# Performance work log

Measured on AMD Instinct MI355X. Metric: run time of the kernel, lower is better.

Reference implementation:

```python
import jax, jax.numpy as jnp
import numpy as np

NUM_EMBEDDINGS = 1024
EMBEDDING_DIM = 64
COMMITMENT_COST = 0.25
N_TOKENS = 262144


def setup_inputs() -> dict:
    key = jax.random.key(0)
    k1, k2 = jax.random.split(key)
    inputs = jax.random.normal(k1, (N_TOKENS, EMBEDDING_DIM), dtype=jnp.float32)
    # torch init: uniform(-1/K, 1/K)
    lim = 1.0 / NUM_EMBEDDINGS
    codebook = jax.random.uniform(k2, (NUM_EMBEDDINGS, EMBEDDING_DIM),
                                  dtype=jnp.float32, minval=-lim, maxval=lim)
    return {"inputs": inputs, "codebook": codebook}


def reference(inputs, codebook):
    # inputs: [N, D] flat tokens, codebook: [K, D]
    x = inputs.reshape(-1, EMBEDDING_DIM)
    distances = (jnp.sum(x * x, axis=1, keepdims=True)
                 + jnp.sum(codebook * codebook, axis=1)
                 - 2.0 * jnp.matmul(x, codebook.T))
    encoding_indices = jnp.argmin(distances, axis=1)[:, None]  # [N, 1]
    # one-hot @ codebook == gather of nearest code vectors
    quantized = codebook[encoding_indices[:, 0]]  # [N, D]
    e_latent_loss = jnp.mean((jax.lax.stop_gradient(quantized) - x) ** 2)
    q_latent_loss = jnp.mean((quantized - jax.lax.stop_gradient(x)) ** 2)
    loss = q_latent_loss + COMMITMENT_COST * e_latent_loss
    # straight-through estimator
    quantized = x + jax.lax.stop_gradient(quantized - x)
    return quantized, loss, encoding_indices
```

## Files before the change

kernel.cpp:

```cpp
#include <hip/hip_runtime.h>
#include <math.h>

#define NTOK   262144
#define DIM    64
#define NCODE  1024
#define LOSSOFF (NTOK*DIM)
#define IDXOFF  (NTOK*DIM + 1)

#define MARGIN 4e-5f
#define RCAP   65536

#define OFF_BC     0
#define OFF_CBHI   1024
#define OFF_CBMID  33792
#define OFF_RCNT   66560
#define OFF_CORR   66561
#define OFF_RLIST  66562
#define OFF_BLK    132098
#define WS_FLOATS  134146

typedef __attribute__((ext_vector_type(8))) short short8;
typedef __attribute__((ext_vector_type(4))) float f32x4;

__device__ __forceinline__ ushort bf16rn(float f) {
    unsigned u = __float_as_uint(f);
    return (ushort)((u + 0x7fffu + ((u >> 16) & 1u)) >> 16);
}
__device__ __forceinline__ float bf16tof(ushort h) {
    return __uint_as_float(((unsigned)h) << 16);
}

__global__ __launch_bounds__(256) void vq_prep_cb(const float* __restrict__ cb,
                                                  float* __restrict__ ws) {
    int c = blockIdx.x * 256 + threadIdx.x;
    if (c == 0) { ((int*)ws)[OFF_RCNT] = 0; ws[OFF_CORR] = 0.f; }
    if (c >= NCODE) return;
    ushort* cbh = (ushort*)(ws + OFF_CBHI);
    ushort* cbm = (ushort*)(ws + OFF_CBMID);
    const float4* p = (const float4*)(cb + (size_t)c * DIM);
    float a0 = 0.f, a1 = 0.f, a2 = 0.f, a3 = 0.f;
#pragma unroll
    for (int i = 0; i < 16; i++) {
        float4 v = p[i];
        a0 = fmaf(v.x, v.x, a0); a1 = fmaf(v.y, v.y, a1);
        a2 = fmaf(v.z, v.z, a2); a3 = fmaf(v.w, v.w, a3);
        ushort4 h, m;
        h.x = bf16rn(v.x); m.x = bf16rn(v.x - bf16tof(h.x));
        h.y = bf16rn(v.y); m.y = bf16rn(v.y - bf16tof(h.y));
        h.z = bf16rn(v.z); m.z = bf16rn(v.z - bf16tof(h.z));
        h.w = bf16rn(v.w); m.w = bf16rn(v.w - bf16tof(h.w));
        ((ushort4*)(cbh + (size_t)c * 64))[i] = h;
        ((ushort4*)(cbm + (size_t)c * 64))[i] = m;
    }
    ws[OFF_BC + c] = (a0 + a1) + (a2 + a3);
}

__global__ __launch_bounds__(256)
__attribute__((amdgpu_waves_per_eu(3)))
void vq_mfma(const float* __restrict__ x,
             const float* __restrict__ cbf,
             float* __restrict__ out,
             float* __restrict__ ws) {
    __shared__ uint4 smem[8][256];
    __shared__ int idxs[128];
    __shared__ float red[4];
    const float* Bc = ws + OFF_BC;
    const ushort* cbh = (const ushort*)(ws + OFF_CBHI);
    const ushort* cbm = (const ushort*)(ws + OFF_CBMID);

    int tid = threadIdx.x, lane = tid & 63, wv = tid >> 6;
    int col = lane & 15, q = lane >> 4, q4 = q * 4;
    int tokb = blockIdx.x * 128 + wv * 32;

    short8 Xhi[2][2], Xmid[2][2];
#pragma unroll
    for (int tt = 0; tt < 2; ++tt) {
        int token = tokb + tt * 16 + col;
        const float* xr = x + (size_t)token * 64;
#pragma unroll
        for (int s = 0; s < 2; ++s) {
            float4 v0 = *(const float4*)(xr + s * 32 + q * 8);
            float4 v1 = *(const float4*)(xr + s * 32 + q * 8 + 4);
            float vv[8] = {v0.x, v0.y, v0.z, v0.w, v1.x, v1.y, v1.z, v1.w};
            short8 hv, mv;
#pragma unroll
            for (int j = 0; j < 8; ++j) {
                ushort h = bf16rn(vv[j]);
                float r = vv[j] - bf16tof(h);
                hv[j] = (short)h; mv[j] = (short)bf16rn(r);
            }
            Xhi[tt][s] = hv; Xmid[tt][s] = mv;
        }
    }

    float best[2][4], sec[2][4];
    int bbase[2][4];
#pragma unroll
    for (int tt = 0; tt < 2; ++tt)
#pragma unroll
        for (int rr = 0; rr < 4; ++rr) {
            best[tt][rr] = 3.4e38f; sec[tt][rr] = 3.4e38f; bbase[tt][rr] = 0;
        }

    int chunk = tid >> 7, e = tid & 127, scode = e >> 3, g = e & 7;
    const ushort* sb0 = (chunk ? cbm : cbh) + (size_t)scode * 64 + g * 8;
    int woff = chunk * 128 + scode * 8 + (g ^ (scode & 7));
    int ro_h0 = col * 8 + ((0 + q) ^ (col & 7));
    int ro_h1 = col * 8 + ((4 + q) ^ (col & 7));
    int ro_m0 = 128 + col * 8 + ((0 + q) ^ (col & 7));
    int ro_m1 = 128 + col * 8 + ((4 + q) ^ (col & 7));

    uint4 r0 = *(const uint4*)(sb0);
    uint4 r1 = *(const uint4*)(sb0 + 1024);
    uint4 r2 = *(const uint4*)(sb0 + 2048);
    uint4 r3 = *(const uint4*)(sb0 + 3072);
    smem[0][woff] = r0; smem[1][woff] = r1;
    smem[2][woff] = r2; smem[3][woff] = r3;
    r0 = *(const uint4*)(sb0 + 4096);
    r1 = *(const uint4*)(sb0 + 5120);
    r2 = *(const uint4*)(sb0 + 6144);
    r3 = *(const uint4*)(sb0 + 7168);
    __syncthreads();

    for (int rd = 0; rd < 16; ++rd) {
        int base = (rd & 1) << 2;
        int nb = 4 - base;
        if (rd < 15) {
            smem[nb + 0][woff] = r0; smem[nb + 1][woff] = r1;
            smem[nb + 2][woff] = r2; smem[nb + 3][woff] = r3;
            if (rd < 14) {
                const ushort* ld = sb0 + (size_t)(rd + 2) * 4096;
                r0 = *(const uint4*)(ld);
                r1 = *(const uint4*)(ld + 1024);
                r2 = *(const uint4*)(ld + 2048);
                r3 = *(const uint4*)(ld + 3072);
            }
        }
#pragma unroll
        for (int sub = 0; sub < 4; ++sub) {
            int c0 = (rd * 4 + sub) * 16;
            float4 bq = *(const float4*)(Bc + c0 + q4);
            short8 Ah0 = *(const short8*)&smem[base + sub][ro_h0];
            short8 Ah1 = *(const short8*)&smem[base + sub][ro_h1];
            short8 Am0 = *(const short8*)&smem[base + sub][ro_m0];
            short8 Am1 = *(const short8*)&smem[base + sub][ro_m1];
            int bv = c0 + q4;
            float bqv[4] = {bq.x, bq.y, bq.z, bq.w};
#pragma unroll
            for (int tt = 0; tt < 2; ++tt) {
                f32x4 acc = {0.f, 0.f, 0.f, 0.f};
                acc = __builtin_amdgcn_mfma_f32_16x16x32_bf16(Ah0, Xhi[tt][0], acc, 0, 0, 0);
                acc = __builtin_amdgcn_mfma_f32_16x16x32_bf16(Ah1, Xhi[tt][1], acc, 0, 0, 0);
                acc = __builtin_amdgcn_mfma_f32_16x16x32_bf16(Ah0, Xmid[tt][0], acc, 0, 0, 0);
                acc = __builtin_amdgcn_mfma_f32_16x16x32_bf16(Ah1, Xmid[tt][1], acc, 0, 0, 0);
                acc = __builtin_amdgcn_mfma_f32_16x16x32_bf16(Am0, Xhi[tt][0], acc, 0, 0, 0);
                acc = __builtin_amdgcn_mfma_f32_16x16x32_bf16(Am1, Xhi[tt][1], acc, 0, 0, 0);
#pragma unroll
                for (int rr = 0; rr < 4; ++rr) {
                    float d = fmaf(-2.f, acc[rr], bqv[rr]);
                    bool lt = d < best[tt][rr];
                    sec[tt][rr] = __builtin_amdgcn_fmed3f(d, best[tt][rr], sec[tt][rr]);
                    best[tt][rr] = fminf(best[tt][rr], d);
                    bbase[tt][rr] = lt ? bv : bbase[tt][rr];
                }
            }
        }
        __syncthreads();
    }

#pragma unroll
    for (int tt = 0; tt < 2; ++tt) {
        float b = best[tt][0], s2 = sec[tt][0];
        int bi = bbase[tt][0];
#pragma unroll
        for (int rr = 1; rr < 4; ++rr) {
            float ob = best[tt][rr];
            int oi = bbase[tt][rr] + rr;
            s2 = fminf(fminf(s2, sec[tt][rr]), fmaxf(b, ob));
            bool lt2 = (ob < b) || (ob == b && oi < bi);
            b = lt2 ? ob : b; bi = lt2 ? oi : bi;
        }
#pragma unroll
        for (int off = 16; off <= 32; off <<= 1) {
            float ob = __shfl_xor(b, off, 64);
            float os = __shfl_xor(s2, off, 64);
            int   oi = __shfl_xor(bi, off, 64);
            s2 = fminf(fminf(s2, os), fmaxf(b, ob));
            bool lt = (ob < b) || (ob == b && oi < bi);
            b = lt ? ob : b; bi = lt ? oi : bi;
        }
        if (lane < 16) {
            int token = tokb + tt * 16 + lane;
            out[IDXOFF + token] = (float)bi;
            idxs[wv * 32 + tt * 16 + lane] = bi;
            if (s2 - b < MARGIN) {
                int pos = atomicAdd((int*)ws + OFF_RCNT, 1);
                if (pos < RCAP) ((int*)ws)[OFF_RLIST + pos] = token;
            }
        }
    }
    __syncthreads();

    float se = 0.f;
    int tokb0 = blockIdx.x * 128;
#pragma unroll
    for (int i = 0; i < 8; ++i) {
        int gi = i * 256 + tid;
        int tok = gi >> 4, qd = gi & 15;
        int ci = idxs[tok];
        float4 xvv = *(const float4*)(x + (size_t)(tokb0 + tok) * 64 + qd * 4);
        float4 qv = *(const float4*)(cbf + (size_t)ci * 64 + qd * 4);
        float d0 = qv.x - xvv.x, d1 = qv.y - xvv.y;
        float d2 = qv.z - xvv.z, d3 = qv.w - xvv.w;
        float4 o;
        o.x = xvv.x + d0; o.y = xvv.y + d1; o.z = xvv.z + d2; o.w = xvv.w + d3;
        *(float4*)(out + (size_t)(tokb0 + tok) * 64 + qd * 4) = o;
        se += d0 * d0 + d1 * d1 + d2 * d2 + d3 * d3;
    }
    for (int off = 32; off; off >>= 1) se += __shfl_down(se, off, 64);
    if (lane == 0) red[wv] = se;
    __syncthreads();
    if (tid == 0) ws[OFF_BLK + blockIdx.x] = (red[0] + red[1]) + (red[2] + red[3]);
}

__global__ __launch_bounds__(256) void vq_refine(const float* __restrict__ x,
                                                 const float* __restrict__ cb,
                                                 float* __restrict__ out,
                                                 float* __restrict__ ws) {
    __shared__ float ctile[128][64];
    __shared__ float xs[8][64];
    __shared__ float As[8];
    __shared__ int   tokid[8], oidx[8], nidx[8];
    __shared__ unsigned long long rkeys[8][128];
    __shared__ float dred[4];

    int cnt = min(((int*)ws)[OFF_RCNT], RCAP);
    if (cnt <= 0) return;
    int ngroups = (cnt + 7) >> 3;
    int tid = threadIdx.x;
    int code = tid & 127, th = tid >> 7;

    for (int grp = blockIdx.x; grp < ngroups; grp += gridDim.x) {
        if (tid < 8) {
            int i = grp * 8 + tid;
            int t = ((int*)ws)[OFF_RLIST + min(i, cnt - 1)];
            tokid[tid] = t;
            oidx[tid] = (int)out[IDXOFF + t];
        }
        __syncthreads();
#pragma unroll
        for (int it = 0; it < 2; ++it) {
            int idx = it * 256 + tid;
            xs[idx >> 6][idx & 63] = x[(size_t)tokid[idx >> 6] * 64 + (idx & 63)];
        }
        __syncthreads();
        if (tid < 8) {
            float a0 = 0.f, a1 = 0.f, a2 = 0.f, a3 = 0.f;
#pragma unroll
            for (int kc = 0; kc < 16; ++kc) {
                float4 xk = *(const float4*)(xs[tid] + kc * 4);
                a0 = fmaf(xk.x, xk.x, a0); a1 = fmaf(xk.y, xk.y, a1);
                a2 = fmaf(xk.z, xk.z, a2); a3 = fmaf(xk.w, xk.w, a3);
            }
            As[tid] = (a0 + a1) + (a2 + a3);
        }

        unsigned long long bk[4] = {~0ull, ~0ull, ~0ull, ~0ull};
        int tb = th * 4;

        for (int pass = 0; pass < 8; ++pass) {
            int cbase = pass * 128;
            __syncthreads();
#pragma unroll
            for (int it = 0; it < 8; ++it) {
                int gi = it * 256 + tid;
                int cc = gi >> 4, qq = gi & 15;
                float4 v = *(const float4*)(cb + (size_t)(cbase + cc) * 64 + qq * 4);
                *(float4*)&ctile[cc][(qq ^ (cc & 15)) * 4] = v;
            }
            __syncthreads();

            float p0 = 0.f, p1 = 0.f, p2 = 0.f, p3 = 0.f;
#pragma unroll
            for (int qq = 0; qq < 16; ++qq) {
                float4 cv = *(const float4*)&ctile[code][(qq ^ (code & 15)) * 4];
                float4 x0 = *(const float4*)(xs[tb + 0] + qq * 4);
                float4 x1 = *(const float4*)(xs[tb + 1] + qq * 4);
                float4 x2 = *(const float4*)(xs[tb + 2] + qq * 4);
                float4 x3 = *(const float4*)(xs[tb + 3] + qq * 4);
                p0 = fmaf(x0.x, cv.x, p0); p0 = fmaf(x0.y, cv.y, p0);
                p0 = fmaf(x0.z, cv.z, p0); p0 = fmaf(x0.w, cv.w, p0);
                p1 = fmaf(x1.x, cv.x, p1); p1 = fmaf(x1.y, cv.y, p1);
                p1 = fmaf(x1.z, cv.z, p1); p1 = fmaf(x1.w, cv.w, p1);
                p2 = fmaf(x2.x, cv.x, p2); p2 = fmaf(x2.y, cv.y, p2);
                p2 = fmaf(x2.z, cv.z, p2); p2 = fmaf(x2.w, cv.w, p2);
                p3 = fmaf(x3.x, cv.x, p3); p3 = fmaf(x3.y, cv.y, p3);
                p3 = fmaf(x3.z, cv.z, p3); p3 = fmaf(x3.w, cv.w, p3);
            }
            float bn = ws[OFF_BC + cbase + code];
            int gcode = cbase + code;
            float pv[4] = {p0, p1, p2, p3};
#pragma unroll
            for (int j = 0; j < 4; ++j) {
                float s = As[tb + j] + bn;
                float d = fmaf(-2.0f, pv[j], s);
                unsigned long long key =
                    (((unsigned long long)__float_as_uint(d)) << 32) | (unsigned)gcode;
                bk[j] = min(bk[j], key);
            }
        }
        __syncthreads();
#pragma unroll
        for (int j = 0; j < 4; ++j) rkeys[tb + j][code] = bk[j];
        __syncthreads();

        int wv2 = tid >> 6, lane = tid & 63;
#pragma unroll
        for (int u = 0; u < 2; ++u) {
            int tt = wv2 * 2 + u;
            unsigned long long k = min(rkeys[tt][lane], rkeys[tt][lane + 64]);
#pragma unroll
            for (int off = 32; off; off >>= 1)
                k = min(k, (unsigned long long)__shfl_xor((long long)k, off, 64));
            if (lane == 0) {
                int ni = (int)(unsigned)(k & 0xffffffffull);
                nidx[tt] = ni;
                if (grp * 8 + tt < cnt) out[IDXOFF + tokid[tt]] = (float)ni;
            }
        }
        __syncthreads();

        float delta = 0.f;
        {
            int tok = tid >> 5, e2 = (tid & 31) * 2;
            if (grp * 8 + tok < cnt) {
                int nw = nidx[tok], od = oidx[tok];
                if (nw != od) {
                    float x0 = xs[tok][e2], x1 = xs[tok][e2 + 1];
                    float qn0 = cb[(size_t)nw * 64 + e2], qn1 = cb[(size_t)nw * 64 + e2 + 1];
                    float qo0 = cb[(size_t)od * 64 + e2], qo1 = cb[(size_t)od * 64 + e2 + 1];
                    float dn0 = qn0 - x0, dn1 = qn1 - x1;
                    float do0 = qo0 - x0, do1 = qo1 - x1;
                    out[(size_t)tokid[tok] * 64 + e2]     = x0 + dn0;
                    out[(size_t)tokid[tok] * 64 + e2 + 1] = x1 + dn1;
                    delta = (dn0 * dn0 + dn1 * dn1) - (do0 * do0 + do1 * do1);
                }
            }
        }
        for (int off = 32; off; off >>= 1) delta += __shfl_down(delta, off, 64);
        if ((tid & 63) == 0) dred[tid >> 6] = delta;
        __syncthreads();
        if (tid == 0) {
            float dsum = (dred[0] + dred[1]) + (dred[2] + dred[3]);
            if (dsum != 0.f) atomicAdd(ws + OFF_CORR, dsum);
        }
        __syncthreads();
    }
}

__global__ __launch_bounds__(256) void vq_loss2(float* __restrict__ out,
                                                const float* __restrict__ ws) {
    const float* blk = ws + OFF_BLK;
    __shared__ double sd[256];
    double s = 0.0;
    for (int i = threadIdx.x; i < 2048; i += 256) s += (double)blk[i];
    sd[threadIdx.x] = s;
    __syncthreads();
    for (int off = 128; off; off >>= 1) {
        if (threadIdx.x < off) sd[threadIdx.x] += sd[threadIdx.x + off];
        __syncthreads();
    }
    if (threadIdx.x == 0) {
        double tot = sd[0] + (double)ws[OFF_CORR];
        out[LOSSOFF] = (float)(1.25 * tot / ((double)NTOK * (double)DIM));
    }
}

extern "C" void kernel_launch(void* const* d_in, const int* in_sizes, int n_in,
                              void* d_out, int out_size, void* d_ws, size_t ws_size,
                              hipStream_t stream) {
    (void)in_sizes; (void)n_in; (void)out_size; (void)ws_size;
    const float* x = (const float*)d_in[0];
    const float* cb = (const float*)d_in[1];
    float* out = (float*)d_out;
    float* ws = (float*)d_ws;

    hipLaunchKernelGGL(vq_prep_cb, dim3(4), dim3(256), 0, stream, cb, ws);
    hipLaunchKernelGGL(vq_mfma, dim3(2048), dim3(256), 0, stream, x, cb, out, ws);
    hipLaunchKernelGGL(vq_refine, dim3(1024), dim3(256), 0, stream, x, cb, out, ws);
    hipLaunchKernelGGL(vq_loss2, dim3(1), dim3(256), 0, stream, out, ws);
}
```

Baseline: 153.9 us.

## Switch distance MFMA from 16x16x32 to 32x32x16 tiles with new LDS layout

Replaces the 16x16x32 bf16 MFMA tiling (two 16-token subtiles per wave) with 32x32x16 MFMAs covering 32 tokens by 32 codes per instruction chain, restructuring the LDS codebook staging, swizzle, and per-lane argmin bookkeeping to match the new accumulator layout. The aim is fewer MFMA issues and LDS fragment reads per code, plus fewer cross-lane shuffles in the final reduction. The trade-off is 16-wide accumulators and 16 best/second/index registers per lane, which raises register pressure under the waves-per-EU hint, and the new index arithmetic has to match the 32x32 output layout exactly.

```diff
diff --git a/kernel.cpp b/kernel.cpp
--- a/kernel.cpp
+++ b/kernel.cpp
@@ -20,7 +20,7 @@
 #define WS_FLOATS  134146
 
 typedef __attribute__((ext_vector_type(8))) short short8;
-typedef __attribute__((ext_vector_type(4))) float f32x4;
+typedef __attribute__((ext_vector_type(16))) float f32x16;
 
 __device__ __forceinline__ ushort bf16rn(float f) {
     unsigned u = __float_as_uint(f);
@@ -61,7 +61,7 @@
              const float* __restrict__ cbf,
              float* __restrict__ out,
              float* __restrict__ ws) {
-    __shared__ uint4 smem[8][256];
+    __shared__ uint4 smem[2][1024];
     __shared__ int idxs[128];
     __shared__ float red[4];
     const float* Bc = ws + OFF_BC;
@@ -69,130 +69,141 @@
     const ushort* cbm = (const ushort*)(ws + OFF_CBMID);
 
     int tid = threadIdx.x, lane = tid & 63, wv = tid >> 6;
-    int col = lane & 15, q = lane >> 4, q4 = q * 4;
+    int col = lane & 31, h = lane >> 5;
     int tokb = blockIdx.x * 128 + wv * 32;
-
-    short8 Xhi[2][2], Xmid[2][2];
-#pragma unroll
-    for (int tt = 0; tt < 2; ++tt) {
-        int token = tokb + tt * 16 + col;
+    int token = tokb + col;
+
+    short8 Xhi[4], Xmid[4];
+    {
         const float* xr = x + (size_t)token * 64;
 #pragma unroll
-        for (int s = 0; s < 2; ++s) {
-            float4 v0 = *(const float4*)(xr + s * 32 + q * 8);
-            float4 v1 = *(const float4*)(xr + s * 32 + q * 8 + 4);
+        for (int kc = 0; kc < 4; ++kc) {
+            float4 v0 = *(const float4*)(xr + kc * 16 + h * 8);
+            float4 v1 = *(const float4*)(xr + kc * 16 + h * 8 + 4);
             float vv[8] = {v0.x, v0.y, v0.z, v0.w, v1.x, v1.y, v1.z, v1.w};
             short8 hv, mv;
 #pragma unroll
             for (int j = 0; j < 8; ++j) {
-                ushort h = bf16rn(vv[j]);
-                float r = vv[j] - bf16tof(h);
-                hv[j] = (short)h; mv[j] = (short)bf16rn(r);
-            }
-            Xhi[tt][s] = hv; Xmid[tt][s] = mv;
-        }
-    }
-
-    float best[2][4], sec[2][4];
-    int bbase[2][4];
-#pragma unroll
-    for (int tt = 0; tt < 2; ++tt)
-#pragma unroll
-        for (int rr = 0; rr < 4; ++rr) {
-            best[tt][rr] = 3.4e38f; sec[tt][rr] = 3.4e38f; bbase[tt][rr] = 0;
-        }
-
-    int chunk = tid >> 7, e = tid & 127, scode = e >> 3, g = e & 7;
-    const ushort* sb0 = (chunk ? cbm : cbh) + (size_t)scode * 64 + g * 8;
-    int woff = chunk * 128 + scode * 8 + (g ^ (scode & 7));
-    int ro_h0 = col * 8 + ((0 + q) ^ (col & 7));
-    int ro_h1 = col * 8 + ((4 + q) ^ (col & 7));
-    int ro_m0 = 128 + col * 8 + ((0 + q) ^ (col & 7));
-    int ro_m1 = 128 + col * 8 + ((4 + q) ^ (col & 7));
-
-    uint4 r0 = *(const uint4*)(sb0);
-    uint4 r1 = *(const uint4*)(sb0 + 1024);
-    uint4 r2 = *(const uint4*)(sb0 + 2048);
-    uint4 r3 = *(const uint4*)(sb0 + 3072);
-    smem[0][woff] = r0; smem[1][woff] = r1;
-    smem[2][woff] = r2; smem[3][woff] = r3;
-    r0 = *(const uint4*)(sb0 + 4096);
-    r1 = *(const uint4*)(sb0 + 5120);
-    r2 = *(const uint4*)(sb0 + 6144);
-    r3 = *(const uint4*)(sb0 + 7168);
+                ushort hb = bf16rn(vv[j]);
+                float r = vv[j] - bf16tof(hb);
+                hv[j] = (short)hb; mv[j] = (short)bf16rn(r);
+            }
+            Xhi[kc] = hv; Xmid[kc] = mv;
+        }
+    }
+
+    float best[16], sec[16];
+    int bbase[16];
+#pragma unroll
+    for (int rr = 0; rr < 16; ++rr) {
+        best[rr] = 3.4e38f; sec[rr] = 3.4e38f; bbase[rr] = 0;
+    }
+
+    const ushort* gsrc[4];
+    int gdst[4];
+#pragma unroll
+    for (int it = 0; it < 4; ++it) {
+        int gi = it * 256 + tid;
+        int tile = gi >> 9, part = (gi >> 8) & 1, code = (gi >> 3) & 31, g = gi & 7;
+        gsrc[it] = (part ? cbm : cbh) + (size_t)(tile * 32 + code) * 64 + g * 8;
+        gdst[it] = tile * 512 + code * 16 + part * 8 + (g ^ (code & 7));
+    }
+    int ro_h[4];
+#pragma unroll
+    for (int kc = 0; kc < 4; ++kc)
+        ro_h[kc] = col * 16 + ((kc * 2 + h) ^ (col & 7));
+
+    uint4 r0 = *(const uint4*)(gsrc[0]);
+    uint4 r1 = *(const uint4*)(gsrc[1]);
+    uint4 r2 = *(const uint4*)(gsrc[2]);
+    uint4 r3 = *(const uint4*)(gsrc[3]);
+    smem[0][gdst[0]] = r0; smem[0][gdst[1]] = r1;
+    smem[0][gdst[2]] = r2; smem[0][gdst[3]] = r3;
+    r0 = *(const uint4*)(gsrc[0] + 4096);
+    r1 = *(const uint4*)(gsrc[1] + 4096);
+    r2 = *(const uint4*)(gsrc[2] + 4096);
+    r3 = *(const uint4*)(gsrc[3] + 4096);
     __syncthreads();
 
     for (int rd = 0; rd < 16; ++rd) {
-        int base = (rd & 1) << 2;
-        int nb = 4 - base;
+        int set = rd & 1;
         if (rd < 15) {
-            smem[nb + 0][woff] = r0; smem[nb + 1][woff] = r1;
-            smem[nb + 2][woff] = r2; smem[nb + 3][woff] = r3;
+            int ns = set ^ 1;
+            smem[ns][gdst[0]] = r0; smem[ns][gdst[1]] = r1;
+            smem[ns][gdst[2]] = r2; smem[ns][gdst[3]] = r3;
             if (rd < 14) {
-                const ushort* ld = sb0 + (size_t)(rd + 2) * 4096;
-                r0 = *(const uint4*)(ld);
-                r1 = *(const uint4*)(ld + 1024);
-                r2 = *(const uint4*)(ld + 2048);
-                r3 = *(const uint4*)(ld + 3072);
-            }
-        }
-#pragma unroll
-        for (int sub = 0; sub < 4; ++sub) {
-            int c0 = (rd * 4 + sub) * 16;
-            float4 bq = *(const float4*)(Bc + c0 + q4);
-            short8 Ah0 = *(const short8*)&smem[base + sub][ro_h0];
-            short8 Ah1 = *(const short8*)&smem[base + sub][ro_h1];
-            short8 Am0 = *(const short8*)&smem[base + sub][ro_m0];
-            short8 Am1 = *(const short8*)&smem[base + sub][ro_m1];
-            int bv = c0 + q4;
-            float bqv[4] = {bq.x, bq.y, bq.z, bq.w};
-#pragma unroll
-            for (int tt = 0; tt < 2; ++tt) {
-                f32x4 acc = {0.f, 0.f, 0.f, 0.f};
-                acc = __builtin_amdgcn_mfma_f32_16x16x32_bf16(Ah0, Xhi[tt][0], acc, 0, 0, 0);
-                acc = __builtin_amdgcn_mfma_f32_16x16x32_bf16(Ah1, Xhi[tt][1], acc, 0, 0, 0);
-                acc = __builtin_amdgcn_mfma_f32_16x16x32_bf16(Ah0, Xmid[tt][0], acc, 0, 0, 0);
-                acc = __builtin_amdgcn_mfma_f32_16x16x32_bf16(Ah1, Xmid[tt][1], acc, 0, 0, 0);
-                acc = __builtin_amdgcn_mfma_f32_16x16x32_bf16(Am0, Xhi[tt][0], acc, 0, 0, 0);
-                acc = __builtin_amdgcn_mfma_f32_16x16x32_bf16(Am1, Xhi[tt][1], acc, 0, 0, 0);
-#pragma unroll
-                for (int rr = 0; rr < 4; ++rr) {
-                    float d = fmaf(-2.f, acc[rr], bqv[rr]);
-                    bool lt = d < best[tt][rr];
-                    sec[tt][rr] = __builtin_amdgcn_fmed3f(d, best[tt][rr], sec[tt][rr]);
-                    best[tt][rr] = fminf(best[tt][rr], d);
-                    bbase[tt][rr] = lt ? bv : bbase[tt][rr];
-                }
-            }
-        }
-        __syncthreads();
-    }
-
-#pragma unroll
-    for (int tt = 0; tt < 2; ++tt) {
-        float b = best[tt][0], s2 = sec[tt][0];
-        int bi = bbase[tt][0];
-#pragma unroll
-        for (int rr = 1; rr < 4; ++rr) {
-            float ob = best[tt][rr];
-            int oi = bbase[tt][rr] + rr;
-            s2 = fminf(fminf(s2, sec[tt][rr]), fmaxf(b, ob));
-            bool lt2 = (ob < b) || (ob == b && oi < bi);
-            b = lt2 ? ob : b; bi = lt2 ? oi : bi;
-        }
-#pragma unroll
-        for (int off = 16; off <= 32; off <<= 1) {
-            float ob = __shfl_xor(b, off, 64);
-            float os = __shfl_xor(s2, off, 64);
-            int   oi = __shfl_xor(bi, off, 64);
-            s2 = fminf(fminf(s2, os), fmaxf(b, ob));
+                size_t off = (size_t)(rd + 2) * 4096;
+                r0 = *(const uint4*)(gsrc[0] + off);
+                r1 = *(const uint4*)(gsrc[1] + off);
+                r2 = *(const uint4*)(gsrc[2] + off);
+                r3 = *(const uint4*)(gsrc[3] + off);
+            }
+        }
+#pragma unroll
+        for (int sub = 0; sub < 2; ++sub) {
+            int c0 = (rd * 2 + sub) * 32;
+            const uint4* tb = &smem[set][sub * 512];
+            short8 Ah0 = __builtin_bit_cast(short8, tb[ro_h[0]]);
+            short8 Ah1 = __builtin_bit_cast(short8, tb[ro_h[1]]);
+            short8 Ah2 = __builtin_bit_cast(short8, tb[ro_h[2]]);
+            short8 Ah3 = __builtin_bit_cast(short8, tb[ro_h[3]]);
+            short8 Am0 = __builtin_bit_cast(short8, tb[ro_h[0] + 8]);
+            short8 Am1 = __builtin_bit_cast(short8, tb[ro_h[1] + 8]);
+            short8 Am2 = __builtin_bit_cast(short8, tb[ro_h[2] + 8]);
+            short8 Am3 = __builtin_bit_cast(short8, tb[ro_h[3] + 8]);
+            float4 bq0 = *(const float4*)(Bc + c0 + 0 * 8 + h * 4);
+            float4 bq1 = *(const float4*)(Bc + c0 + 1 * 8 + h * 4);
+            float4 bq2 = *(const float4*)(Bc + c0 + 2 * 8 + h * 4);
+            float4 bq3 = *(const float4*)(Bc + c0 + 3 * 8 + h * 4);
+            float bqa[16] = {bq0.x, bq0.y, bq0.z, bq0.w,
+                             bq1.x, bq1.y, bq1.z, bq1.w,
+                             bq2.x, bq2.y, bq2.z, bq2.w,
+                             bq3.x, bq3.y, bq3.z, bq3.w};
+            f32x16 acc = {0.f};
+            acc = __builtin_amdgcn_mfma_f32_32x32x16_bf16(Ah0, Xhi[0], acc, 0, 0, 0);
+            acc = __builtin_amdgcn_mfma_f32_32x32x16_bf16(Ah1, Xhi[1], acc, 0, 0, 0);
+            acc = __builtin_amdgcn_mfma_f32_32x32x16_bf16(Ah2, Xhi[2], acc, 0, 0, 0);
+            acc = __builtin_amdgcn_mfma_f32_32x32x16_bf16(Ah3, Xhi[3], acc, 0, 0, 0);
+            acc = __builtin_amdgcn_mfma_f32_32x32x16_bf16(Ah0, Xmid[0], acc, 0, 0, 0);
+            acc = __builtin_amdgcn_mfma_f32_32x32x16_bf16(Ah1, Xmid[1], acc, 0, 0, 0);
+            acc = __builtin_amdgcn_mfma_f32_32x32x16_bf16(Ah2, Xmid[2], acc, 0, 0, 0);
+            acc = __builtin_amdgcn_mfma_f32_32x32x16_bf16(Ah3, Xmid[3], acc, 0, 0, 0);
+            acc = __builtin_amdgcn_mfma_f32_32x32x16_bf16(Am0, Xhi[0], acc, 0, 0, 0);
+            acc = __builtin_amdgcn_mfma_f32_32x32x16_bf16(Am1, Xhi[1], acc, 0, 0, 0);
+            acc = __builtin_amdgcn_mfma_f32_32x32x16_bf16(Am2, Xhi[2], acc, 0, 0, 0);
+            acc = __builtin_amdgcn_mfma_f32_32x32x16_bf16(Am3, Xhi[3], acc, 0, 0, 0);
+#pragma unroll
+            for (int rr = 0; rr < 16; ++rr) {
+                float d = fmaf(-2.f, acc[rr], bqa[rr]);
+                bool lt = d < best[rr];
+                sec[rr] = __builtin_amdgcn_fmed3f(d, best[rr], sec[rr]);
+                best[rr] = fminf(best[rr], d);
+                bbase[rr] = lt ? c0 : bbase[rr];
+            }
+        }
+        __syncthreads();
+    }
+
+    {
+        float b = best[0], s2 = sec[0];
+        int bi = bbase[0] + 4 * h;
+#pragma unroll
+        for (int rr = 1; rr < 16; ++rr) {
+            float ob = best[rr];
+            int oi = bbase[rr] + (rr & 3) + 8 * (rr >> 2) + 4 * h;
+            s2 = fminf(fminf(s2, sec[rr]), fmaxf(b, ob));
             bool lt = (ob < b) || (ob == b && oi < bi);
             b = lt ? ob : b; bi = lt ? oi : bi;
         }
-        if (lane < 16) {
-            int token = tokb + tt * 16 + lane;
+        float ob = __shfl_xor(b, 32, 64);
+        float os = __shfl_xor(s2, 32, 64);
+        int   oi = __shfl_xor(bi, 32, 64);
+        s2 = fminf(fminf(s2, os), fmaxf(b, ob));
+        bool lt = (ob < b) || (ob == b && oi < bi);
+        b = lt ? ob : b; bi = lt ? oi : bi;
+        if (lane < 32) {
             out[IDXOFF + token] = (float)bi;
-            idxs[wv * 32 + tt * 16 + lane] = bi;
+            idxs[wv * 32 + lane] = bi;
             if (s2 - b < MARGIN) {
                 int pos = atomicAdd((int*)ws + OFF_RCNT, 1);
                 if (pos < RCAP) ((int*)ws)[OFF_RLIST + pos] = token;
```

New measurement: 211.4 us, median of 2. 1.37x slower.

## Stream codebook tiles directly into LDS with global_load_lds and pre-swizzled layout

Applied to the files above, without the earlier changes.

The codebook staging path no longer goes global→registers→LDS. It now issues direct global-to-LDS async loads (global_load_lds, 16 bytes per lane) into the double buffer. To keep the bank-conflict-free XOR layout, the swizzle moves into the prep kernel, which stores the bf16 hi/mid codebook already permuted. This frees VGPRs and removes the ds_write traffic. In exchange it relies on the LDS write ordering and barriers being enough for asynchronous loads, and the row mapping per wave changes from the old per-thread scheme.

```diff
diff --git a/kernel.cpp b/kernel.cpp
--- a/kernel.cpp
+++ b/kernel.cpp
@@ -22,6 +22,10 @@
 typedef __attribute__((ext_vector_type(8))) short short8;
 typedef __attribute__((ext_vector_type(4))) float f32x4;
 
+#define GLOAD_LDS(g, l) __builtin_amdgcn_global_load_lds(                    \
+    (const __attribute__((address_space(1))) void*)(g),                     \
+    (__attribute__((address_space(3))) void*)(l), 16, 0, 0)
+
 __device__ __forceinline__ ushort bf16rn(float f) {
     unsigned u = __float_as_uint(f);
     return (ushort)((u + 0x7fffu + ((u >> 16) & 1u)) >> 16);
@@ -38,6 +42,7 @@
     ushort* cbh = (ushort*)(ws + OFF_CBHI);
     ushort* cbm = (ushort*)(ws + OFF_CBMID);
     const float4* p = (const float4*)(cb + (size_t)c * DIM);
+    int sw = (c & 7) << 1;
     float a0 = 0.f, a1 = 0.f, a2 = 0.f, a3 = 0.f;
 #pragma unroll
     for (int i = 0; i < 16; i++) {
@@ -49,8 +54,8 @@
         h.y = bf16rn(v.y); m.y = bf16rn(v.y - bf16tof(h.y));
         h.z = bf16rn(v.z); m.z = bf16rn(v.z - bf16tof(h.z));
         h.w = bf16rn(v.w); m.w = bf16rn(v.w - bf16tof(h.w));
-        ((ushort4*)(cbh + (size_t)c * 64))[i] = h;
-        ((ushort4*)(cbm + (size_t)c * 64))[i] = m;
+        ((ushort4*)(cbh + (size_t)c * 64))[i ^ sw] = h;
+        ((ushort4*)(cbm + (size_t)c * 64))[i ^ sw] = m;
     }
     ws[OFF_BC + c] = (a0 + a1) + (a2 + a3);
 }
@@ -102,39 +107,25 @@
             best[tt][rr] = 3.4e38f; sec[tt][rr] = 3.4e38f; bbase[tt][rr] = 0;
         }
 
-    int chunk = tid >> 7, e = tid & 127, scode = e >> 3, g = e & 7;
-    const ushort* sb0 = (chunk ? cbm : cbh) + (size_t)scode * 64 + g * 8;
-    int woff = chunk * 128 + scode * 8 + (g ^ (scode & 7));
+    const ushort* wsrc = (wv < 2 ? cbh : cbm) + (size_t)(wv & 1) * 512 + lane * 8;
     int ro_h0 = col * 8 + ((0 + q) ^ (col & 7));
     int ro_h1 = col * 8 + ((4 + q) ^ (col & 7));
     int ro_m0 = 128 + col * 8 + ((0 + q) ^ (col & 7));
     int ro_m1 = 128 + col * 8 + ((4 + q) ^ (col & 7));
 
-    uint4 r0 = *(const uint4*)(sb0);
-    uint4 r1 = *(const uint4*)(sb0 + 1024);
-    uint4 r2 = *(const uint4*)(sb0 + 2048);
-    uint4 r3 = *(const uint4*)(sb0 + 3072);
-    smem[0][woff] = r0; smem[1][woff] = r1;
-    smem[2][woff] = r2; smem[3][woff] = r3;
-    r0 = *(const uint4*)(sb0 + 4096);
-    r1 = *(const uint4*)(sb0 + 5120);
-    r2 = *(const uint4*)(sb0 + 6144);
-    r3 = *(const uint4*)(sb0 + 7168);
+#pragma unroll
+    for (int t = 0; t < 4; ++t)
+        GLOAD_LDS(wsrc + t * 1024, &smem[t][wv * 64]);
     __syncthreads();
 
     for (int rd = 0; rd < 16; ++rd) {
         int base = (rd & 1) << 2;
-        int nb = 4 - base;
         if (rd < 15) {
-            smem[nb + 0][woff] = r0; smem[nb + 1][woff] = r1;
-            smem[nb + 2][woff] = r2; smem[nb + 3][woff] = r3;
-            if (rd < 14) {
-                const ushort* ld = sb0 + (size_t)(rd + 2) * 4096;
-                r0 = *(const uint4*)(ld);
-                r1 = *(const uint4*)(ld + 1024);
-                r2 = *(const uint4*)(ld + 2048);
-                r3 = *(const uint4*)(ld + 3072);
-            }
+            int nb = 4 - base;
+            const ushort* ts = wsrc + (size_t)(rd + 1) * 4096;
+#pragma unroll
+            for (int t = 0; t < 4; ++t)
+                GLOAD_LDS(ts + t * 1024, &smem[nb + t][wv * 64]);
         }
 #pragma unroll
         for (int sub = 0; sub < 4; ++sub) {
```

Measured after the change: 156.0 us. About the same (+1.4%).
